# Kernel optimization log

Hardware: AMD Instinct MI355X
Metric: run time of the kernel (lower is better)

Reference implementation:

```python
import jax, jax.numpy as jnp
import numpy as np

BS, N, FEAT = 4, 4096, 64
LN_EPS = 1e-5


def setup_inputs() -> dict:
    key = jax.random.key(0)
    k1, k2, k3 = jax.random.split(key, 3)
    positions = jax.random.normal(k1, (BS, N, 3), dtype=jnp.float32)
    # nn.Linear(n_point, feature_dim): weight (FEAT, N), bias (FEAT,)
    W = jax.random.normal(k2, (FEAT, N), dtype=jnp.float32) * (1.0 / np.sqrt(N))
    b = jax.random.normal(k3, (FEAT,), dtype=jnp.float32) * 0.02
    gamma = jnp.ones((FEAT,), dtype=jnp.float32)
    beta = jnp.zeros((FEAT,), dtype=jnp.float32)
    return {"positions": positions, "W": W, "b": b, "gamma": gamma, "beta": beta}


def reference(positions, W, b, gamma, beta):
    # all-pairs squared distances: (bs, N, N)
    diff = positions[:, :, None, :] - positions[:, None, :, :]  # (bs,N,N,3)
    sq = jnp.sum(diff * diff, axis=-1)                          # (bs,N,N)
    # safe sqrt (diagonal is exactly 0)
    safe = jnp.where(sq > 0, sq, 1.0)
    dist = jnp.where(sq > 0, jnp.sqrt(safe), 0.0)               # (bs,N,N)
    # Linear(N -> FEAT)
    x = jnp.einsum('bnm,fm->bnf', dist, W) + b                  # (bs,N,FEAT)
    # LayerNorm over last dim (biased variance, eps=1e-5)
    mu = jnp.mean(x, axis=-1, keepdims=True)
    var = jnp.mean((x - mu) ** 2, axis=-1, keepdims=True)
    xn = (x - mu) / jnp.sqrt(var + LN_EPS) * gamma + beta
    # SiLU
    return xn * jax.nn.sigmoid(xn)
```

## Files before the change

kernel.cpp:

```cpp
#include <hip/hip_runtime.h>


typedef float f32x4 __attribute__((ext_vector_type(4)));
typedef __bf16 bf16x8 __attribute__((ext_vector_type(8)));

union BF8 { bf16x8 v; uint4 u; };

#define N_PTS 4096
#define FEATD 64
#define BK 256
#define NCH (N_PTS / BK)

__global__ void wconv_kernel(const float* __restrict__ W,
                             unsigned short* __restrict__ Wbt) {
  int gid = blockIdx.x * blockDim.x + threadIdx.x;
  int f = gid >> 9, m8 = gid & 511;
  const float4* src = (const float4*)(W + (size_t)f * N_PTS + m8 * 8);
  float4 a = src[0], b = src[1];
  BF8 o;
  o.v[0] = (__bf16)a.x; o.v[1] = (__bf16)a.y; o.v[2] = (__bf16)a.z; o.v[3] = (__bf16)a.w;
  o.v[4] = (__bf16)b.x; o.v[5] = (__bf16)b.y; o.v[6] = (__bf16)b.z; o.v[7] = (__bf16)b.w;
  ((uint4*)Wbt)[(size_t)m8 * 64 + f] = o.u;
}

__device__ __forceinline__ void load_lds16(const void* g, void* l) {
  __builtin_amdgcn_global_load_lds(
      (const __attribute__((address_space(1))) void*)g,
      (__attribute__((address_space(3))) void*)l, 16, 0, 0);
}

__global__ __launch_bounds__(1024, 4) void frp_kernel(
    const float* __restrict__ pos, const float* __restrict__ W,
    const float* __restrict__ bias, const float* __restrict__ gamma,
    const float* __restrict__ beta, const unsigned short* __restrict__ Wbt,
    float* __restrict__ out) {
  __shared__ uint4 Wbuf[2][2048];
  __shared__ __align__(16) float Px[N_PTS];
  __shared__ __align__(16) float Py[N_PTS];
  __shared__ __align__(16) float Pz[N_PTS];

  const int tid = threadIdx.x;
  const int lane = tid & 63;
  const int wave = tid >> 6;
  const int rs  = wave & 1;
  const int ksl = wave >> 1;
  const int fx = lane & 15;
  const int q = lane >> 4;

  const int batch = blockIdx.x >> 6;
  const int nb = (blockIdx.x & 63) * 64;
  const float* posB = pos + (size_t)batch * N_PTS * 3;

  {
    const float4* p4 = (const float4*)posB;
    float4 f0 = p4[tid * 3 + 0];
    float4 f1 = p4[tid * 3 + 1];
    float4 f2 = p4[tid * 3 + 2];
    ((float4*)Px)[tid] = make_float4(f0.x, f0.w, f1.z, f2.y);
    ((float4*)Py)[tid] = make_float4(f0.y, f1.x, f1.w, f2.z);
    ((float4*)Pz)[tid] = make_float4(f0.z, f1.y, f2.x, f2.w);
  }

  const bool useWb = (Wbt != nullptr);

  auto stageW = [&](int c, int b) {
#pragma unroll
    for (int it = 0; it < 2; ++it) {
      int gi = it * 1024 + tid;
      if (useWb) {
        load_lds16(Wbt + ((size_t)c * 2048 + gi) * 8, &Wbuf[b][gi]);
      } else {
        int g = gi >> 6, f = gi & 63;
        const float4* src = (const float4*)(W + (size_t)f * N_PTS + c * BK + g * 8);
        float4 a = src[0], b2 = src[1];
        BF8 o;
        o.v[0] = (__bf16)a.x;  o.v[1] = (__bf16)a.y;  o.v[2] = (__bf16)a.z;  o.v[3] = (__bf16)a.w;
        o.v[4] = (__bf16)b2.x; o.v[5] = (__bf16)b2.y; o.v[6] = (__bf16)b2.z; o.v[7] = (__bf16)b2.w;
        Wbuf[b][gi] = o.u;
      }
    }
  };

  f32x4 acc[2][4];
#pragma unroll
  for (int a = 0; a < 2; ++a)
#pragma unroll
    for (int t = 0; t < 4; ++t) acc[a][t] = (f32x4){0.f, 0.f, 0.f, 0.f};

  stageW(0, 0);
  __syncthreads();

  const int nrow0 = nb + rs * 32 + fx;
  const float px0 = Px[nrow0],      py0 = Py[nrow0],      pz0 = Pz[nrow0];
  const float px1 = Px[nrow0 + 16], py1 = Py[nrow0 + 16], pz1 = Pz[nrow0 + 16];

  const int g8 = ksl * 4 + q;

  for (int c = 0; c < NCH; ++c) {
    if (c + 1 < NCH) stageW(c + 1, (c + 1) & 1);
    const uint4* Wcur = Wbuf[c & 1];
    const int m4 = c * 64 + g8 * 2;
    f32x4 xa = ((const f32x4*)Px)[m4], xb = ((const f32x4*)Px)[m4 + 1];
    f32x4 ya = ((const f32x4*)Py)[m4], yb = ((const f32x4*)Py)[m4 + 1];
    f32x4 za = ((const f32x4*)Pz)[m4], zb = ((const f32x4*)Pz)[m4 + 1];

    bf16x8 af0, af1;
    {
      f32x4 dx = xa - px0, dy = ya - py0, dz = za - pz0;
      f32x4 sq = dx * dx + dy * dy + dz * dz;
#pragma unroll
      for (int j = 0; j < 4; ++j) af0[j] = (__bf16)__builtin_amdgcn_sqrtf(sq[j]);
      dx = xb - px0; dy = yb - py0; dz = zb - pz0;
      sq = dx * dx + dy * dy + dz * dz;
#pragma unroll
      for (int j = 0; j < 4; ++j) af0[4 + j] = (__bf16)__builtin_amdgcn_sqrtf(sq[j]);
      dx = xa - px1; dy = ya - py1; dz = za - pz1;
      sq = dx * dx + dy * dy + dz * dz;
#pragma unroll
      for (int j = 0; j < 4; ++j) af1[j] = (__bf16)__builtin_amdgcn_sqrtf(sq[j]);
      dx = xb - px1; dy = yb - py1; dz = zb - pz1;
      sq = dx * dx + dy * dy + dz * dz;
#pragma unroll
      for (int j = 0; j < 4; ++j) af1[4 + j] = (__bf16)__builtin_amdgcn_sqrtf(sq[j]);
    }
#pragma unroll
    for (int t = 0; t < 4; ++t) {
      BF8 bw;
      bw.u = Wcur[g8 * 64 + t * 16 + fx];
      acc[0][t] = __builtin_amdgcn_mfma_f32_16x16x32_bf16(af0, bw.v, acc[0][t], 0, 0, 0);
      acc[1][t] = __builtin_amdgcn_mfma_f32_16x16x32_bf16(af1, bw.v, acc[1][t], 0, 0, 0);
    }
    __syncthreads();
  }

  f32x4* mbv = (f32x4*)Wbuf;
  __syncthreads();
  if (ksl >= 4) {
    int w = (ksl - 4) * 2 + rs;
#pragma unroll
    for (int a = 0; a < 2; ++a)
#pragma unroll
      for (int t = 0; t < 4; ++t)
        mbv[w * 512 + (a * 4 + t) * 64 + lane] = acc[a][t];
  }
  __syncthreads();
  if (ksl < 4) {
    int w = ksl * 2 + rs;
#pragma unroll
    for (int a = 0; a < 2; ++a)
#pragma unroll
      for (int t = 0; t < 4; ++t)
        acc[a][t] += mbv[w * 512 + (a * 4 + t) * 64 + lane];
  }
  __syncthreads();
  if (ksl >= 1 && ksl < 4) {
    int w = (ksl - 1) * 2 + rs;
#pragma unroll
    for (int a = 0; a < 2; ++a)
#pragma unroll
      for (int t = 0; t < 4; ++t)
        mbv[w * 512 + (a * 4 + t) * 64 + lane] = acc[a][t];
  }
  __syncthreads();
  if (ksl == 0) {
#pragma unroll
    for (int s = 0; s < 3; ++s)
#pragma unroll
      for (int a = 0; a < 2; ++a)
#pragma unroll
        for (int t = 0; t < 4; ++t)
          acc[a][t] += mbv[(s * 2 + rs) * 512 + (a * 4 + t) * 64 + lane];

    float bb[4], gg[4], be[4];
#pragma unroll
    for (int t = 0; t < 4; ++t) {
      bb[t] = bias[t * 16 + fx];
      gg[t] = gamma[t * 16 + fx];
      be[t] = beta[t * 16 + fx];
    }
    float* outB = out + ((size_t)batch * N_PTS + nb + rs * 32) * FEATD;
#pragma unroll
    for (int a = 0; a < 2; ++a) {
#pragma unroll
      for (int r = 0; r < 4; ++r) {
        float x[4], d[4];
#pragma unroll
        for (int t = 0; t < 4; ++t) x[t] = acc[a][t][r] + bb[t];
        float s = x[0] + x[1] + x[2] + x[3];
        s += __shfl_xor(s, 1); s += __shfl_xor(s, 2);
        s += __shfl_xor(s, 4); s += __shfl_xor(s, 8);
        float mu = s * (1.f / 64.f);
        float v = 0.f;
#pragma unroll
        for (int t = 0; t < 4; ++t) { d[t] = x[t] - mu; v += d[t] * d[t]; }
        v += __shfl_xor(v, 1); v += __shfl_xor(v, 2);
        v += __shfl_xor(v, 4); v += __shfl_xor(v, 8);
        float rstd = __builtin_amdgcn_rsqf(v * (1.f / 64.f) + 1e-5f);
        float* orow = outB + (a * 16 + q * 4 + r) * FEATD;
#pragma unroll
        for (int t = 0; t < 4; ++t) {
          float xn = d[t] * rstd * gg[t] + be[t];
          float y = xn * (1.f / (1.f + __expf(-xn)));
          orow[t * 16 + fx] = y;
        }
      }
    }
  }
}

extern "C" void kernel_launch(void* const* d_in, const int* in_sizes, int n_in,
                              void* d_out, int out_size, void* d_ws, size_t ws_size,
                              hipStream_t stream) {
  const float* pos   = (const float*)d_in[0];
  const float* W     = (const float*)d_in[1];
  const float* bias  = (const float*)d_in[2];
  const float* gamma = (const float*)d_in[3];
  const float* beta  = (const float*)d_in[4];
  float* out = (float*)d_out;

  const size_t wb_bytes = (size_t)FEATD * N_PTS * sizeof(unsigned short);
  int use_ws = (d_ws != nullptr && ws_size >= wb_bytes);
  unsigned short* Wbt = use_ws ? (unsigned short*)d_ws : nullptr;

  if (use_ws) {
    wconv_kernel<<<dim3((FEATD * N_PTS / 8) / 256), dim3(256), 0, stream>>>(W, Wbt);
  }
  frp_kernel<<<dim3(256), dim3(1024), 0, stream>>>(pos, W, bias, gamma, beta, Wbt, out);
}
```

Baseline: 87.06 us.

## Move position SoA transpose to prep kernel and use smaller 32-row blocks

Position transposition into SoA layout moves into a combined prep kernel alongside the W bf16 conversion, writing to workspace, so the main kernel no longer stages all positions in LDS. The main kernel now uses 512-thread blocks covering 32 rows each, with 512 blocks instead of 256, and reads key coordinates directly from global memory. This cuts LDS use and per-block setup and doubles the block count, at the cost of more global/L2 traffic for positions and twice as many reads of W per output row. The K-split reduction is restructured into a 3-stage tree across 8 waves.

```diff
diff --git a/kernel.cpp b/kernel.cpp
--- a/kernel.cpp
+++ b/kernel.cpp
@@ -9,18 +9,34 @@
 #define N_PTS 4096
 #define FEATD 64
 #define BK 256
-#define NCH (N_PTS / BK)
-
-__global__ void wconv_kernel(const float* __restrict__ W,
-                             unsigned short* __restrict__ Wbt) {
-  int gid = blockIdx.x * blockDim.x + threadIdx.x;
-  int f = gid >> 9, m8 = gid & 511;
-  const float4* src = (const float4*)(W + (size_t)f * N_PTS + m8 * 8);
-  float4 a = src[0], b = src[1];
-  BF8 o;
-  o.v[0] = (__bf16)a.x; o.v[1] = (__bf16)a.y; o.v[2] = (__bf16)a.z; o.v[3] = (__bf16)a.w;
-  o.v[4] = (__bf16)b.x; o.v[5] = (__bf16)b.y; o.v[6] = (__bf16)b.z; o.v[7] = (__bf16)b.w;
-  ((uint4*)Wbt)[(size_t)m8 * 64 + f] = o.u;
+#define NCH 16
+
+__global__ void prep_kernel(const float* __restrict__ W,
+                            const float* __restrict__ pos,
+                            unsigned short* __restrict__ Wbt,
+                            float* __restrict__ Pt) {
+  int b = blockIdx.x, t = threadIdx.x;
+  if (b < 128) {
+    int gid = b * 256 + t;
+    int f = gid >> 9, m8 = gid & 511;
+    const float4* src = (const float4*)(W + (size_t)f * N_PTS + m8 * 8);
+    float4 a = src[0], bb = src[1];
+    BF8 o;
+    o.v[0] = (__bf16)a.x;  o.v[1] = (__bf16)a.y;  o.v[2] = (__bf16)a.z;  o.v[3] = (__bf16)a.w;
+    o.v[4] = (__bf16)bb.x; o.v[5] = (__bf16)bb.y; o.v[6] = (__bf16)bb.z; o.v[7] = (__bf16)bb.w;
+    ((uint4*)Wbt)[(size_t)m8 * 64 + f] = o.u;
+  } else {
+    int bb = b - 128;
+    int batch = bb >> 2, qtr = bb & 3;
+    const float4* p4 = (const float4*)(pos + ((size_t)batch * N_PTS + qtr * 1024) * 3);
+    float4 f0 = p4[t * 3 + 0], f1 = p4[t * 3 + 1], f2 = p4[t * 3 + 2];
+    float4* Px = (float4*)(Pt + (size_t)(0 * 4 + batch) * N_PTS) + qtr * 256;
+    float4* Py = (float4*)(Pt + (size_t)(1 * 4 + batch) * N_PTS) + qtr * 256;
+    float4* Pz = (float4*)(Pt + (size_t)(2 * 4 + batch) * N_PTS) + qtr * 256;
+    Px[t] = make_float4(f0.x, f0.w, f1.z, f2.y);
+    Py[t] = make_float4(f0.y, f1.x, f1.w, f2.z);
+    Pz[t] = make_float4(f0.z, f1.y, f2.x, f2.w);
+  }
 }
 
 __device__ __forceinline__ void load_lds16(const void* g, void* l) {
@@ -29,45 +45,45 @@
       (__attribute__((address_space(3))) void*)l, 16, 0, 0);
 }
 
-__global__ __launch_bounds__(1024, 4) void frp_kernel(
+__global__ __launch_bounds__(512, 4) void frp_kernel(
     const float* __restrict__ pos, const float* __restrict__ W,
     const float* __restrict__ bias, const float* __restrict__ gamma,
     const float* __restrict__ beta, const unsigned short* __restrict__ Wbt,
-    float* __restrict__ out) {
+    const float* __restrict__ Pt, float* __restrict__ out) {
   __shared__ uint4 Wbuf[2][2048];
-  __shared__ __align__(16) float Px[N_PTS];
-  __shared__ __align__(16) float Py[N_PTS];
-  __shared__ __align__(16) float Pz[N_PTS];
 
   const int tid = threadIdx.x;
   const int lane = tid & 63;
   const int wave = tid >> 6;
-  const int rs  = wave & 1;
-  const int ksl = wave >> 1;
   const int fx = lane & 15;
   const int q = lane >> 4;
 
-  const int batch = blockIdx.x >> 6;
-  const int nb = (blockIdx.x & 63) * 64;
+  const int batch = blockIdx.x >> 7;
+  const int rb = (blockIdx.x & 127) * 32;
   const float* posB = pos + (size_t)batch * N_PTS * 3;
-
+  const bool useWs = (Wbt != nullptr);
+
+  const float* PxG = Pt + (size_t)(0 * 4 + batch) * N_PTS;
+  const float* PyG = Pt + (size_t)(1 * 4 + batch) * N_PTS;
+  const float* PzG = Pt + (size_t)(2 * 4 + batch) * N_PTS;
+
+  float px0, py0, pz0, px1, py1, pz1;
   {
-    const float4* p4 = (const float4*)posB;
-    float4 f0 = p4[tid * 3 + 0];
-    float4 f1 = p4[tid * 3 + 1];
-    float4 f2 = p4[tid * 3 + 2];
-    ((float4*)Px)[tid] = make_float4(f0.x, f0.w, f1.z, f2.y);
-    ((float4*)Py)[tid] = make_float4(f0.y, f1.x, f1.w, f2.z);
-    ((float4*)Pz)[tid] = make_float4(f0.z, f1.y, f2.x, f2.w);
-  }
-
-  const bool useWb = (Wbt != nullptr);
+    int n0 = rb + fx;
+    if (useWs) {
+      px0 = PxG[n0];      py0 = PyG[n0];      pz0 = PzG[n0];
+      px1 = PxG[n0 + 16]; py1 = PyG[n0 + 16]; pz1 = PzG[n0 + 16];
+    } else {
+      px0 = posB[n0 * 3];        py0 = posB[n0 * 3 + 1];        pz0 = posB[n0 * 3 + 2];
+      px1 = posB[(n0 + 16) * 3]; py1 = posB[(n0 + 16) * 3 + 1]; pz1 = posB[(n0 + 16) * 3 + 2];
+    }
+  }
 
   auto stageW = [&](int c, int b) {
 #pragma unroll
-    for (int it = 0; it < 2; ++it) {
-      int gi = it * 1024 + tid;
-      if (useWb) {
+    for (int it = 0; it < 4; ++it) {
+      int gi = it * 512 + tid;
+      if (useWs) {
         load_lds16(Wbt + ((size_t)c * 2048 + gi) * 8, &Wbuf[b][gi]);
       } else {
         int g = gi >> 6, f = gi & 63;
@@ -90,39 +106,40 @@
   stageW(0, 0);
   __syncthreads();
 
-  const int nrow0 = nb + rs * 32 + fx;
-  const float px0 = Px[nrow0],      py0 = Py[nrow0],      pz0 = Pz[nrow0];
-  const float px1 = Px[nrow0 + 16], py1 = Py[nrow0 + 16], pz1 = Pz[nrow0 + 16];
-
-  const int g8 = ksl * 4 + q;
+  const int g8 = wave * 4 + q;
 
   for (int c = 0; c < NCH; ++c) {
     if (c + 1 < NCH) stageW(c + 1, (c + 1) & 1);
     const uint4* Wcur = Wbuf[c & 1];
-    const int m4 = c * 64 + g8 * 2;
-    f32x4 xa = ((const f32x4*)Px)[m4], xb = ((const f32x4*)Px)[m4 + 1];
-    f32x4 ya = ((const f32x4*)Py)[m4], yb = ((const f32x4*)Py)[m4 + 1];
-    f32x4 za = ((const f32x4*)Pz)[m4], zb = ((const f32x4*)Pz)[m4 + 1];
+
+    float kx[8], ky[8], kz[8];
+    if (useWs) {
+      const int m4 = c * 64 + g8 * 2;
+      f32x4 xa = ((const f32x4*)PxG)[m4], xb = ((const f32x4*)PxG)[m4 + 1];
+      f32x4 ya = ((const f32x4*)PyG)[m4], yb = ((const f32x4*)PyG)[m4 + 1];
+      f32x4 za = ((const f32x4*)PzG)[m4], zb = ((const f32x4*)PzG)[m4 + 1];
+#pragma unroll
+      for (int j = 0; j < 4; ++j) {
+        kx[j] = xa[j]; ky[j] = ya[j]; kz[j] = za[j];
+        kx[4 + j] = xb[j]; ky[4 + j] = yb[j]; kz[4 + j] = zb[j];
+      }
+    } else {
+      const float* pk = posB + ((size_t)c * BK + g8 * 8) * 3;
+#pragma unroll
+      for (int j = 0; j < 8; ++j) {
+        kx[j] = pk[j * 3]; ky[j] = pk[j * 3 + 1]; kz[j] = pk[j * 3 + 2];
+      }
+    }
 
     bf16x8 af0, af1;
-    {
-      f32x4 dx = xa - px0, dy = ya - py0, dz = za - pz0;
-      f32x4 sq = dx * dx + dy * dy + dz * dz;
-#pragma unroll
-      for (int j = 0; j < 4; ++j) af0[j] = (__bf16)__builtin_amdgcn_sqrtf(sq[j]);
-      dx = xb - px0; dy = yb - py0; dz = zb - pz0;
-      sq = dx * dx + dy * dy + dz * dz;
-#pragma unroll
-      for (int j = 0; j < 4; ++j) af0[4 + j] = (__bf16)__builtin_amdgcn_sqrtf(sq[j]);
-      dx = xa - px1; dy = ya - py1; dz = za - pz1;
-      sq = dx * dx + dy * dy + dz * dz;
-#pragma unroll
-      for (int j = 0; j < 4; ++j) af1[j] = (__bf16)__builtin_amdgcn_sqrtf(sq[j]);
-      dx = xb - px1; dy = yb - py1; dz = zb - pz1;
-      sq = dx * dx + dy * dy + dz * dz;
-#pragma unroll
-      for (int j = 0; j < 4; ++j) af1[4 + j] = (__bf16)__builtin_amdgcn_sqrtf(sq[j]);
-    }
+#pragma unroll
+    for (int j = 0; j < 8; ++j) {
+      float dx = kx[j] - px0, dy = ky[j] - py0, dz = kz[j] - pz0;
+      af0[j] = (__bf16)__builtin_amdgcn_sqrtf(dx * dx + dy * dy + dz * dz);
+      dx = kx[j] - px1; dy = ky[j] - py1; dz = kz[j] - pz1;
+      af1[j] = (__bf16)__builtin_amdgcn_sqrtf(dx * dx + dy * dy + dz * dz);
+    }
+
 #pragma unroll
     for (int t = 0; t < 4; ++t) {
       BF8 bw;
@@ -134,43 +151,33 @@
   }
 
   f32x4* mbv = (f32x4*)Wbuf;
-  __syncthreads();
-  if (ksl >= 4) {
-    int w = (ksl - 4) * 2 + rs;
+  auto wr = [&](int rg) {
 #pragma unroll
     for (int a = 0; a < 2; ++a)
 #pragma unroll
       for (int t = 0; t < 4; ++t)
-        mbv[w * 512 + (a * 4 + t) * 64 + lane] = acc[a][t];
-  }
-  __syncthreads();
-  if (ksl < 4) {
-    int w = ksl * 2 + rs;
+        mbv[rg * 512 + (a * 4 + t) * 64 + lane] = acc[a][t];
+  };
+  auto rd = [&](int rg) {
 #pragma unroll
     for (int a = 0; a < 2; ++a)
 #pragma unroll
       for (int t = 0; t < 4; ++t)
-        acc[a][t] += mbv[w * 512 + (a * 4 + t) * 64 + lane];
-  }
-  __syncthreads();
-  if (ksl >= 1 && ksl < 4) {
-    int w = (ksl - 1) * 2 + rs;
-#pragma unroll
-    for (int a = 0; a < 2; ++a)
-#pragma unroll
-      for (int t = 0; t < 4; ++t)
-        mbv[w * 512 + (a * 4 + t) * 64 + lane] = acc[a][t];
-  }
-  __syncthreads();
-  if (ksl == 0) {
-#pragma unroll
-    for (int s = 0; s < 3; ++s)
-#pragma unroll
-      for (int a = 0; a < 2; ++a)
-#pragma unroll
-        for (int t = 0; t < 4; ++t)
-          acc[a][t] += mbv[(s * 2 + rs) * 512 + (a * 4 + t) * 64 + lane];
-
+        acc[a][t] += mbv[rg * 512 + (a * 4 + t) * 64 + lane];
+  };
+  if (wave >= 4) wr(wave - 4);
+  __syncthreads();
+  if (wave < 4) rd(wave);
+  __syncthreads();
+  if (wave == 2 || wave == 3) wr(wave - 2);
+  __syncthreads();
+  if (wave < 2) rd(wave);
+  __syncthreads();
+  if (wave == 1) wr(0);
+  __syncthreads();
+
+  if (wave == 0) {
+    rd(0);
     float bb[4], gg[4], be[4];
 #pragma unroll
     for (int t = 0; t < 4; ++t) {
@@ -178,7 +185,7 @@
       gg[t] = gamma[t * 16 + fx];
       be[t] = beta[t * 16 + fx];
     }
-    float* outB = out + ((size_t)batch * N_PTS + nb + rs * 32) * FEATD;
+    float* outB = out + ((size_t)batch * N_PTS + rb) * FEATD;
 #pragma unroll
     for (int a = 0; a < 2; ++a) {
 #pragma unroll
@@ -219,11 +226,13 @@
   float* out = (float*)d_out;
 
   const size_t wb_bytes = (size_t)FEATD * N_PTS * sizeof(unsigned short);
-  int use_ws = (d_ws != nullptr && ws_size >= wb_bytes);
+  const size_t pt_bytes = (size_t)3 * 4 * N_PTS * sizeof(float);
+  int use_ws = (d_ws != nullptr && ws_size >= wb_bytes + pt_bytes);
   unsigned short* Wbt = use_ws ? (unsigned short*)d_ws : nullptr;
+  float* Pt = use_ws ? (float*)((char*)d_ws + wb_bytes) : nullptr;
 
   if (use_ws) {
-    wconv_kernel<<<dim3((FEATD * N_PTS / 8) / 256), dim3(256), 0, stream>>>(W, Wbt);
-  }
-  frp_kernel<<<dim3(256), dim3(1024), 0, stream>>>(pos, W, bias, gamma, beta, Wbt, out);
-}
+    prep_kernel<<<dim3(144), dim3(256), 0, stream>>>(W, pos, Wbt, Pt);
+  }
+  frp_kernel<<<dim3(512), dim3(512), 0, stream>>>(pos, W, bias, gamma, beta, Wbt, Pt, out);
+}
```

Measured after the change: 95.34 us. 1.1x slower.
